# Kernel tuning notes

Hardware: AMD Instinct MI355X
Metric: run time of the kernel (lower is better)

## Reference

```python
import jax, jax.numpy as jnp
import numpy as np

TRIM = 0.2
ALPHA = 0.5
SCALES = 4
B, H, W = 64, 384, 512


def _normalize_robust(x, mask):
    # per-sample masked median shift, masked mean-abs-dev scale (MiDaS SSI norm)
    b = x.shape[0]
    xf = x.reshape(b, -1)
    mf = mask.reshape(b, -1)
    n = mf.sum(axis=1)                                   # valid count per row
    s = jnp.sort(jnp.where(mf, xf, jnp.inf), axis=1)     # masked-out -> +inf, sorted to tail
    med_idx = jnp.maximum((n - 1) // 2, 0)               # torch.median = lower median
    shift = jnp.take_along_axis(s, med_idx[:, None], axis=1)      # [b,1]
    scale = (jnp.abs(xf - shift) * mf).sum(axis=1) / n.astype(xf.dtype)
    return ((xf - shift) / scale[:, None]).reshape(x.shape)


def _gradient_loss(pred, targ):
    mask = targ > 0
    gx = jnp.abs(pred[:, :, 1:] - pred[:, :, :-1])
    gy = jnp.abs(pred[:, 1:, :] - pred[:, :-1, :])
    mx = (mask[:, :, 1:] & mask[:, :, :-1]).astype(pred.dtype)
    my = (mask[:, 1:, :] & mask[:, :-1, :]).astype(pred.dtype)
    norm = mask.sum(axis=(1, 2))
    loss = (gx * mx).sum(axis=(1, 2)) + (gy * my).sum(axis=(1, 2))
    valid = norm > 0
    loss = jnp.where(valid, loss / jnp.maximum(norm, 1).astype(pred.dtype), 0.0)
    return loss.mean()


def _multiscale_gradient_loss(pred, targ):
    total = jnp.asarray(0.0, pred.dtype)
    for scale in range(SCALES):
        step = 2 ** scale
        total = total + _gradient_loss(pred[:, ::step, ::step], targ[:, ::step, ::step])
    return total


def _trimmed_mae(pred, targ):
    b = pred.shape[0]
    p = pred.reshape(b, -1)
    t = targ.reshape(b, -1)
    n_px = p.shape[1]
    mask = t > 0
    res = jnp.where(mask, jnp.abs(p - t), 0.0)
    # NOTE: faithful to source, which indexes the UNSORTED res at max_index
    # (sorted_res is computed then never used for the threshold).
    max_index = (~mask).sum(axis=1) + int((1.0 - TRIM) * n_px)
    max_index = jnp.minimum(max_index, n_px - 1)
    thr = jnp.take_along_axis(res, max_index[:, None], axis=1)    # [b,1]
    res = jnp.where(res > thr, 0.0, res)
    norm = 2 * mask.sum(axis=1)
    valid = norm > 0
    loss = res.sum(axis=1)
    loss = jnp.where(valid, loss / jnp.maximum(norm, 1).astype(p.dtype), 0.0)
    return loss.mean()


def setup_inputs() -> dict:
    key = jax.random.key(0)
    kp, kt = jax.random.split(key)
    prediction = jax.random.normal(kp, (B, H, W), dtype=jnp.float32)
    target = jax.random.normal(kt, (B, H, W), dtype=jnp.float32)
    return {"prediction": prediction, "target": target}


def reference(prediction, target):
    mask = target > 0
    pred_n = _normalize_robust(prediction, mask)
    targ_n = _normalize_robust(target, mask)
    loss = _trimmed_mae(pred_n, targ_n)
    loss = loss + ALPHA * _multiscale_gradient_loss(pred_n, targ_n)
    return loss
```

## Files before the change

### kernel.cpp

```cpp
#include <hip/hip_runtime.h>
#include <stdint.h>

#define B 64
#define H 384
#define W 512
#define NPX (H*W)
#define TRIM_IDX 157286
#define RPW 8

#define NB1 4096
#define NBA 2048
#define NBB 512
#define CAPW 256
#define NSLOT 64
#define CAPD 8192

#define HIST_U32 (2*B*NB1)
#define ACC_OFF  HIST_U32
#define N_OFF    (ACC_OFF + 0)
#define MS_OFF   (ACC_OFF + 64)
#define TS_OFF   (ACC_OFF + 256)
#define GS_OFF   (ACC_OFF + 320)
#define TSUM_OFF (ACC_OFF + 576)
#define SB_OFF   (ACC_OFF + 704)
#define OVF_OFF  (ACC_OFF + 832)
#define ZERO_U32 (ACC_OFF + 1024)
#define K_OFF    (ACC_OFF + 1024)
#define PFX_OFF  (ACC_OFF + 1152)
#define EQ_OFF   (ACC_OFF + 1280)
#define SH_OFF   (ACC_OFF + 1408)
#define RS_OFF   (ACC_OFF + 1536)
#define THR_OFF  (ACC_OFF + 1664)
#define C2_OFF   (ACC_OFF + 1728)
#define CNT1_OFF (ACC_OFF + 1792)
#define CNTW_OFF (ACC_OFF + 1920)
#define FIX_U32  (ACC_OFF + 1920 + 2*B*NSLOT)
#define BUF_OFF  FIX_U32

__device__ __forceinline__ uint32_t fmap(float f) {
    uint32_t b = __float_as_uint(f);
    return (b & 0x80000000u) ? ~b : (b | 0x80000000u);
}
__device__ __forceinline__ float funmap(uint32_t u) {
    uint32_t b = (u & 0x80000000u) ? (u & 0x7fffffffu) : ~u;
    return __uint_as_float(b);
}

__global__ void __launch_bounds__(256) hist1_kernel(const float* __restrict__ pred,
                                                    const float* __restrict__ targ,
                                                    uint32_t* __restrict__ ws) {
    __shared__ uint32_t lh[2 * NB1];
    const int b = blockIdx.y;
    for (int i = threadIdx.x; i < 2 * NB1; i += 256) lh[i] = 0;
    __syncthreads();
    const float4* pb = (const float4*)(pred + (size_t)b * NPX);
    const float4* tb = (const float4*)(targ + (size_t)b * NPX);
    const int tid = blockIdx.x * 256 + threadIdx.x;
    uint32_t nloc = 0;
    float sump = 0.f, sumt = 0.f;
    #pragma unroll
    for (int r = 0; r < 3; r++) {
        float4 ta0 = tb[tid + (4*r+0)*4096], ta1 = tb[tid + (4*r+1)*4096];
        float4 ta2 = tb[tid + (4*r+2)*4096], ta3 = tb[tid + (4*r+3)*4096];
        float4 pa0 = pb[tid + (4*r+0)*4096], pa1 = pb[tid + (4*r+1)*4096];
        float4 pa2 = pb[tid + (4*r+2)*4096], pa3 = pb[tid + (4*r+3)*4096];
        float tA[16] = {ta0.x,ta0.y,ta0.z,ta0.w, ta1.x,ta1.y,ta1.z,ta1.w,
                        ta2.x,ta2.y,ta2.z,ta2.w, ta3.x,ta3.y,ta3.z,ta3.w};
        float pA[16] = {pa0.x,pa0.y,pa0.z,pa0.w, pa1.x,pa1.y,pa1.z,pa1.w,
                        pa2.x,pa2.y,pa2.z,pa2.w, pa3.x,pa3.y,pa3.z,pa3.w};
        #pragma unroll
        for (int e = 0; e < 16; e++) {
            float t = tA[e];
            if (t > 0.f) {
                float p = pA[e];
                nloc++; sumt += t; sump += p;
                atomicAdd(&lh[fmap(p) >> 20], 1u);
                atomicAdd(&lh[NB1 + (fmap(t) >> 20)], 1u);
            }
        }
    }
    __syncthreads();
    uint32_t* hist = ws;
    for (int i = threadIdx.x; i < 2 * NB1; i += 256) {
        uint32_t v = lh[i];
        if (v) {
            int which = i >> 12, bin = i & (NB1 - 1);
            atomicAdd(&hist[(size_t)(which * B + b) * NB1 + bin], v);
        }
    }
    for (int off = 32; off; off >>= 1) {
        nloc += __shfl_down(nloc, off, 64);
        sump += __shfl_down(sump, off, 64);
        sumt += __shfl_down(sumt, off, 64);
    }
    if ((threadIdx.x & 63) == 0) {
        if (nloc) atomicAdd(ws + N_OFF + b, nloc);
        atomicAdd(((float*)(ws + TSUM_OFF)) + b, sump);
        atomicAdd(((float*)(ws + TSUM_OFF)) + B + b, sumt);
    }
}

__global__ void select1_kernel(uint32_t* __restrict__ ws) {
    const int b = blockIdx.x, which = blockIdx.y;
    const uint32_t* h = ws + (size_t)(which * B + b) * NB1;
    const uint32_t k = (ws[N_OFF + b] - 1u) >> 1;
    const int t = threadIdx.x;
    uint32_t mysum = 0;
    #pragma unroll
    for (int i = 0; i < 16; i++) mysum += h[t * 16 + i];
    __shared__ uint32_t s[256];
    s[t] = mysum;
    __syncthreads();
    for (int off = 1; off < 256; off <<= 1) {
        uint32_t add = (t >= off) ? s[t - off] : 0u;
        __syncthreads();
        s[t] += add;
        __syncthreads();
    }
    uint32_t incl = s[t], excl = incl - mysum;
    if (k >= excl && k < incl) {
        uint32_t c = excl, bin = 0, newk = 0, e = 0;
        for (int i = 0; i < 16; i++) {
            uint32_t hv = h[t * 16 + i];
            if (k < c + hv) { bin = t * 16 + i; newk = k - c; e = hv; break; }
            c += hv;
        }
        ws[PFX_OFF + which * B + b] = bin;
        ws[K_OFF + which * B + b] = newk;
        ws[CNT1_OFF + which * B + b] = e;
    }
}

__global__ void __launch_bounds__(256) collect2_kernel(const float* __restrict__ pred,
                                                       const float* __restrict__ targ,
                                                       uint32_t* __restrict__ ws, int capw) {
    const int b = blockIdx.y;
    const int t = threadIdx.x;
    const int lane = t & 63;
    const int slot = (blockIdx.x << 2) + (t >> 6);
    const uint32_t pfxp = ws[PFX_OFF + b];
    const uint32_t pfxt = ws[PFX_OFF + B + b];
    const float4* pb = (const float4*)(pred + (size_t)b * NPX);
    const float4* tb = (const float4*)(targ + (size_t)b * NPX);
    const int tid = blockIdx.x * 256 + t;
    float* bufp = ((float*)(ws + BUF_OFF)) + ((size_t)b * NSLOT + slot) * capw;
    float* buft = ((float*)(ws + BUF_OFF)) + (((size_t)B + b) * NSLOT + slot) * capw;
    float sbp = 0.f, sbt = 0.f;
    uint32_t wp = 0, wt = 0;
    #pragma unroll
    for (int r = 0; r < 3; r++) {
        float4 ta0 = tb[tid + (4*r+0)*4096], ta1 = tb[tid + (4*r+1)*4096];
        float4 ta2 = tb[tid + (4*r+2)*4096], ta3 = tb[tid + (4*r+3)*4096];
        float4 pa0 = pb[tid + (4*r+0)*4096], pa1 = pb[tid + (4*r+1)*4096];
        float4 pa2 = pb[tid + (4*r+2)*4096], pa3 = pb[tid + (4*r+3)*4096];
        float tA[16] = {ta0.x,ta0.y,ta0.z,ta0.w, ta1.x,ta1.y,ta1.z,ta1.w,
                        ta2.x,ta2.y,ta2.z,ta2.w, ta3.x,ta3.y,ta3.z,ta3.w};
        float pA[16] = {pa0.x,pa0.y,pa0.z,pa0.w, pa1.x,pa1.y,pa1.z,pa1.w,
                        pa2.x,pa2.y,pa2.z,pa2.w, pa3.x,pa3.y,pa3.z,pa3.w};
        uint32_t mbp = 0, mbt = 0;
        #pragma unroll
        for (int e = 0; e < 16; e++) {
            float tv = tA[e], pv = pA[e];
            bool msk = tv > 0.f;
            uint32_t u1p = fmap(pv) >> 20, u1t = fmap(tv) >> 20;
            if (msk && u1p < pfxp) sbp += pv;
            if (msk && u1t < pfxt) sbt += tv;
            if (msk && u1p == pfxp) mbp |= (1u << e);
            if (msk && u1t == pfxt) mbt |= (1u << e);
        }
        uint32_t packed = (uint32_t)__popc(mbp) | ((uint32_t)__popc(mbt) << 16);
        uint32_t scan = packed;
        #pragma unroll
        for (int off = 1; off < 64; off <<= 1) {
            uint32_t v = (uint32_t)__shfl_up((int)scan, off, 64);
            if (lane >= off) scan += v;
        }
        uint32_t tot = (uint32_t)__shfl((int)scan, 63, 64);
        uint32_t exl = scan - packed;
        uint32_t op = wp + (exl & 0xFFFFu);
        uint32_t ot = wt + (exl >> 16);
        if (mbp | mbt) {
            #pragma unroll
            for (int e = 0; e < 16; e++) {
                if ((mbp >> e) & 1u) { if (op < (uint32_t)capw) bufp[op] = pA[e]; op++; }
                if ((mbt >> e) & 1u) { if (ot < (uint32_t)capw) buft[ot] = tA[e]; ot++; }
            }
        }
        wp += tot & 0xFFFFu;
        wt += tot >> 16;
    }
    if (lane == 0) {
        ws[CNTW_OFF + b * NSLOT + slot] = wp;
        ws[CNTW_OFF + (B + b) * NSLOT + slot] = wt;
        if (wp > (uint32_t)capw) ws[OVF_OFF + b] = 1u;
        if (wt > (uint32_t)capw) ws[OVF_OFF + B + b] = 1u;
    }
    for (int off = 32; off; off >>= 1) {
        sbp += __shfl_down(sbp, off, 64);
        sbt += __shfl_down(sbt, off, 64);
    }
    if (lane == 0) {
        atomicAdd(((float*)(ws + SB_OFF)) + b, sbp);
        atomicAdd(((float*)(ws + SB_OFF)) + B + b, sbt);
    }
}

__global__ void small3_kernel(const float* __restrict__ pred,
                              const float* __restrict__ targ,
                              uint32_t* __restrict__ ws, int capw) {
    const int b = blockIdx.x, which = blockIdx.y;
    const int t = threadIdx.x;
    __shared__ float dense[CAPD];
    __shared__ uint32_t cnt[NBA];
    __shared__ float fsm[NBA];
    __shared__ uint32_t sc[256];
    __shared__ float sfl[256];
    __shared__ uint32_t scnt[NSLOT], soff[NSLOT];
    __shared__ uint32_t r_bin, r_k;
    __shared__ float r_f;
    const uint32_t pfx1 = ws[PFX_OFF + which * B + b];
    const uint32_t k1 = ws[K_OFF + which * B + b];
    const uint32_t C = ws[CNT1_OFF + which * B + b];
    const bool fast = (capw > 0) && (ws[OVF_OFF + which * B + b] == 0u) && (C <= (uint32_t)CAPD);
    const uint32_t* cw = ws + CNTW_OFF + (which * B + b) * NSLOT;
    const float* bufb = ((const float*)(ws + BUF_OFF)) + ((size_t)which * B + b) * NSLOT * capw;
    const float* Tp = targ + (size_t)b * NPX;
    const float* Pp = pred + (size_t)b * NPX;

    uint32_t myc = 0;
    if (fast && t < NSLOT) myc = cw[t];
    sc[t] = myc;
    __syncthreads();
    for (int off = 1; off < NSLOT; off <<= 1) {
        uint32_t a = (t >= off) ? sc[t - off] : 0u;
        __syncthreads();
        sc[t] += a;
        __syncthreads();
    }
    if (t < NSLOT) { scnt[t] = myc; soff[t] = sc[t] - myc; }
    __syncthreads();
    if (fast) {
        const int s = t >> 2;
        const float* sb_ = bufb + (size_t)s * capw;
        const uint32_t n = scnt[s], o = soff[s];
        for (uint32_t j = (uint32_t)(t & 3); j < n; j += 4) dense[o + j] = sb_[j];
    }
    __syncthreads();

    for (int i = t; i < NBA; i += 256) { cnt[i] = 0; fsm[i] = 0.f; }
    __syncthreads();
    if (fast) {
        for (uint32_t j = t; j < C; j += 256) {
            float v = dense[j];
            uint32_t u = fmap(v), mb = (u >> 9) & (NBA - 1u);
            atomicAdd(&cnt[mb], 1u); atomicAdd(&fsm[mb], v);
        }
    } else {
        for (int j = t; j < NPX; j += 256) {
            float tvv = Tp[j];
            if (tvv > 0.f) {
                float v = (which == 0) ? Pp[j] : tvv;
                uint32_t u = fmap(v);
                if ((u >> 20) == pfx1) {
                    uint32_t mb = (u >> 9) & (NBA - 1u);
                    atomicAdd(&cnt[mb], 1u); atomicAdd(&fsm[mb], v);
                }
            }
        }
    }
    __syncthreads();
    {
        uint32_t ms = 0; float mf = 0.f;
        #pragma unroll
        for (int i = 0; i < 8; i++) { ms += cnt[t * 8 + i]; mf += fsm[t * 8 + i]; }
        sc[t] = ms; sfl[t] = mf;
        __syncthreads();
        for (int off = 1; off < 256; off <<= 1) {
            uint32_t a = (t >= off) ? sc[t - off] : 0u;
            float af = (t >= off) ? sfl[t - off] : 0.f;
            __syncthreads();
            sc[t] += a; sfl[t] += af;
            __syncthreads();
        }
        uint32_t incl = sc[t], excl = incl - ms;
        float fx = sfl[t] - mf;
        if (k1 >= excl && k1 < incl) {
            uint32_t c = excl, bin = 0, nk = 0; float f = fx;
            for (int i = 0; i < 8; i++) {
                uint32_t hv = cnt[t * 8 + i];
                if (k1 < c + hv) { bin = t * 8 + i; nk = k1 - c; break; }
                c += hv; f += fsm[t * 8 + i];
            }
            r_bin = bin; r_k = nk; r_f = f;
        }
    }
    __syncthreads();
    const uint32_t mid_sel = r_bin, k2 = r_k;
    const float fbelowA = r_f;
    __syncthreads();
    for (int i = t; i < NBB; i += 256) { cnt[i] = 0; fsm[i] = 0.f; }
    __syncthreads();
    if (fast) {
        for (uint32_t j = t; j < C; j += 256) {
            float v = dense[j];
            uint32_t u = fmap(v);
            if (((u >> 9) & (NBA - 1u)) == mid_sel) {
                uint32_t lb = u & (NBB - 1u);
                atomicAdd(&cnt[lb], 1u); atomicAdd(&fsm[lb], v);
            }
        }
    } else {
        for (int j = t; j < NPX; j += 256) {
            float tvv = Tp[j];
            if (tvv > 0.f) {
                float v = (which == 0) ? Pp[j] : tvv;
                uint32_t u = fmap(v);
                if ((u >> 20) == pfx1 && ((u >> 9) & (NBA - 1u)) == mid_sel) {
                    uint32_t lb = u & (NBB - 1u);
                    atomicAdd(&cnt[lb], 1u); atomicAdd(&fsm[lb], v);
                }
            }
        }
    }
    __syncthreads();
    {
        uint32_t ms = 0; float mf = 0.f;
        #pragma unroll
        for (int i = 0; i < 2; i++) { ms += cnt[t * 2 + i]; mf += fsm[t * 2 + i]; }
        sc[t] = ms; sfl[t] = mf;
        __syncthreads();
        for (int off = 1; off < 256; off <<= 1) {
            uint32_t a = (t >= off) ? sc[t - off] : 0u;
            float af = (t >= off) ? sfl[t - off] : 0.f;
            __syncthreads();
            sc[t] += a; sfl[t] += af;
            __syncthreads();
        }
        uint32_t incl = sc[t], excl = incl - ms;
        float fx = sfl[t] - mf;
        if (k2 >= excl && k2 < incl) {
            uint32_t c = excl, bin = 0, nk = 0, e = 0; float f = fx;
            for (int i = 0; i < 2; i++) {
                uint32_t hv = cnt[t * 2 + i];
                if (k2 < c + hv) { bin = t * 2 + i; nk = k2 - c; e = hv; break; }
                c += hv; f += fsm[t * 2 + i];
            }
            uint32_t u = (pfx1 << 20) | (mid_sel << 9) | bin;
            ((float*)(ws + SH_OFF))[which * B + b] = funmap(u);
            ws[K_OFF + which * B + b] = nk;
            ws[EQ_OFF + which * B + b] = e;
            ((float*)(ws + SB_OFF))[which * B + b] += fbelowA + f;
        }
    }
}

__global__ void param_kernel(const float* __restrict__ pred,
                             const float* __restrict__ targ,
                             uint32_t* __restrict__ ws) {
    const int b = threadIdx.x;
    if (b >= B) return;
    const uint32_t n = ws[N_OFF + b];
    const uint32_t k0 = (n - 1u) >> 1;
    float med[2], rs[2];
    uint32_t nab[2];
    #pragma unroll
    for (int w = 0; w < 2; w++) {
        float m = ((const float*)(ws + SH_OFF))[w * B + b];
        uint32_t k3 = ws[K_OFF + w * B + b];
        uint32_t e = ws[EQ_OFF + w * B + b];
        float SBv = ((const float*)(ws + SB_OFF))[w * B + b];
        float ST = ((const float*)(ws + TSUM_OFF))[w * B + b];
        uint32_t CB = k0 - k3;
        uint32_t na = n - CB - e;
        float Sab = ST - SBv - (float)e * m;
        float absdev = (Sab - (float)na * m) + ((float)CB * m - SBv);
        float scale = absdev / (float)n;
        med[w] = m; nab[w] = na;
        rs[w] = 1.f / scale;
        ((float*)(ws + RS_OFF))[w * B + b] = rs[w];
    }
    uint32_t c2 = nab[1];
    ws[C2_OFF + b] = c2;
    uint32_t mi = (uint32_t)NPX - c2 + (uint32_t)TRIM_IDX;
    if (mi > (uint32_t)(NPX - 1)) mi = NPX - 1;
    float p = pred[(size_t)b * NPX + mi];
    float t = targ[(size_t)b * NPX + mi];
    float pn = (p - med[0]) * rs[0], tn = (t - med[1]) * rs[1];
    ((float*)(ws + THR_OFF))[b] = (tn > 0.f) ? fabsf(pn - tn) : 0.f;
}

__global__ void __launch_bounds__(256) loss_kernel(const float* __restrict__ pred,
                                                   const float* __restrict__ targ,
                                                   uint32_t* __restrict__ ws) {
    const int wid = (blockIdx.x << 2) + (threadIdx.x >> 6);
    const int b = wid / (H / RPW);
    const int s0 = (wid - b * (H / RPW)) * RPW;
    const int l = threadIdx.x & 63;
    const int col = l << 3;
    const float sp = ((const float*)(ws + SH_OFF))[b];
    const float st = ((const float*)(ws + SH_OFF))[B + b];
    const float rp = ((const float*)(ws + RS_OFF))[b];
    const float rt = ((const float*)(ws + RS_OFF))[B + b];
    const float thr = ((const float*)(ws + THR_OFF))[b];
    const float* Pp = pred + (size_t)b * NPX;
    const float* Tp = targ + (size_t)b * NPX;

    const bool g1 = s0 >= 1, g2 = s0 >= 2, g4 = s0 >= 4, g8 = s0 >= 8;
    float rT[2][8], rPN[2][8];
    {
        const int roA = (g1 ? (s0 - 1) : s0) * W + col;
        const int roB = (g2 ? (s0 - 2) : s0) * W + col;
        float4 a0 = *(const float4*)(Tp + roA), a1 = *(const float4*)(Tp + roA + 4);
        float4 b0 = *(const float4*)(Pp + roA), b1 = *(const float4*)(Pp + roA + 4);
        float4 c0 = *(const float4*)(Tp + roB), c1 = *(const float4*)(Tp + roB + 4);
        float4 d0 = *(const float4*)(Pp + roB), d1 = *(const float4*)(Pp + roB + 4);
        float ta[8] = {a0.x,a0.y,a0.z,a0.w,a1.x,a1.y,a1.z,a1.w};
        float pa[8] = {b0.x,b0.y,b0.z,b0.w,b1.x,b1.y,b1.z,b1.w};
        float tc[8] = {c0.x,c0.y,c0.z,c0.w,c1.x,c1.y,c1.z,c1.w};
        float pc[8] = {d0.x,d0.y,d0.z,d0.w,d1.x,d1.y,d1.z,d1.w};
        #pragma unroll
        for (int k = 0; k < 8; k++) {
            rT[1][k] = ta[k]; rPN[1][k] = (pa[k] - sp) * rp;
            rT[0][k] = tc[k]; rPN[0][k] = (pc[k] - sp) * rp;
        }
    }

    float tl = 0.f, gl0 = 0.f, gl1 = 0.f, gl2 = 0.f, gl3 = 0.f;
    uint32_t mc = 0;

    #pragma unroll
    for (int it = 0; it < RPW; ++it) {
        const int ro = (s0 + it) * W + col;
        const int cur = it & 1, prv = cur ^ 1;
        float4 a0 = *(const float4*)(Tp + ro), a1 = *(const float4*)(Tp + ro + 4);
        float4 b0 = *(const float4*)(Pp + ro), b1 = *(const float4*)(Pp + ro + 4);
        float t[8] = {a0.x,a0.y,a0.z,a0.w,a1.x,a1.y,a1.z,a1.w};
        float p[8] = {b0.x,b0.y,b0.z,b0.w,b1.x,b1.y,b1.z,b1.w};
        float t4a = 0.f, t4b = 0.f, p4a = 0.f, p4b = 0.f, t8a = 0.f, p8a = 0.f;
        if (it == 0) {
            const int ro4 = g4 ? ro - 4 * W : ro;
            t4a = Tp[ro4]; t4b = Tp[ro4 + 4]; p4a = Pp[ro4]; p4b = Pp[ro4 + 4];
            const int ro8 = g8 ? ro - 8 * W : ro;
            t8a = Tp[ro8]; p8a = Pp[ro8];
        }
        if (it == 4) {
            const int ro4 = ro - 4 * W;
            t4a = Tp[ro4]; t4b = Tp[ro4 + 4]; p4a = Pp[ro4]; p4b = Pp[ro4 + 4];
        }
        float pn[8]; bool m[8];
        #pragma unroll
        for (int k = 0; k < 8; k++) { pn[k] = (p[k] - sp) * rp; m[k] = t[k] > st; }

        #pragma unroll
        for (int k = 0; k < 8; k++) {
            if (m[k]) {
                float tn = (t[k] - st) * rt;
                float r = fabsf(pn[k] - tn);
                if (r <= thr) tl += r;
            }
        }
        float t7p = __shfl_up(t[7], 1), pn7p = __shfl_up(pn[7], 1);
        if (l > 0 && m[0] && t7p > st) gl0 += fabsf(pn[0] - pn7p);
        #pragma unroll
        for (int k = 1; k < 8; k++) if (m[k] && m[k - 1]) gl0 += fabsf(pn[k] - pn[k - 1]);
        if (it > 0 || g1) {
            #pragma unroll
            for (int k = 0; k < 8; k++)
                if (m[k] && rT[prv][k] > st) gl0 += fabsf(pn[k] - rPN[prv][k]);
        }
        if ((it & 1) == 0) {
            float t6p = __shfl_up(t[6], 1), pn6p = __shfl_up(pn[6], 1);
            mc += (uint32_t)m[0] + m[2] + m[4] + m[6];
            if (l > 0 && m[0] && t6p > st) gl1 += fabsf(pn[0] - pn6p);
            if (m[2] && m[0]) gl1 += fabsf(pn[2] - pn[0]);
            if (m[4] && m[2]) gl1 += fabsf(pn[4] - pn[2]);
            if (m[6] && m[4]) gl1 += fabsf(pn[6] - pn[4]);
            if (it >= 2 || g2) {
                if (m[0] && rT[cur][0] > st) gl1 += fabsf(pn[0] - rPN[cur][0]);
                if (m[2] && rT[cur][2] > st) gl1 += fabsf(pn[2] - rPN[cur][2]);
                if (m[4] && rT[cur][4] > st) gl1 += fabsf(pn[4] - rPN[cur][4]);
                if (m[6] && rT[cur][6] > st) gl1 += fabsf(pn[6] - rPN[cur][6]);
            }
            if ((it & 3) == 0) {
                float t4p = __shfl_up(t[4], 1), pn4p = __shfl_up(pn[4], 1);
                mc += ((uint32_t)m[0] + m[4]) << 11;
                if (l > 0 && m[0] && t4p > st) gl2 += fabsf(pn[0] - pn4p);
                if (m[4] && m[0]) gl2 += fabsf(pn[4] - pn[0]);
                if (it == 4 || g4) {
                    if (m[0] && t4a > st) gl2 += fabsf(pn[0] - (p4a - sp) * rp);
                    if (m[4] && t4b > st) gl2 += fabsf(pn[4] - (p4b - sp) * rp);
                }
                if (it == 0) {
                    float t0p = __shfl_up(t[0], 1), pn0p = __shfl_up(pn[0], 1);
                    mc += ((uint32_t)m[0]) << 22;
                    if (l > 0 && m[0] && t0p > st) gl3 += fabsf(pn[0] - pn0p);
                    if (g8 && m[0] && t8a > st) gl3 += fabsf(pn[0] - (p8a - sp) * rp);
                }
            }
        }
        #pragma unroll
        for (int k = 0; k < 8; k++) { rT[cur][k] = t[k]; rPN[cur][k] = pn[k]; }
    }

    for (int off = 32; off; off >>= 1) {
        tl  += __shfl_down(tl, off, 64);
        gl0 += __shfl_down(gl0, off, 64);
        gl1 += __shfl_down(gl1, off, 64);
        gl2 += __shfl_down(gl2, off, 64);
        gl3 += __shfl_down(gl3, off, 64);
        mc  += __shfl_down(mc, off, 64);
    }
    if (l == 0) {
        float* gs = (float*)(ws + GS_OFF);
        atomicAdd(((float*)(ws + TS_OFF)) + b, tl);
        atomicAdd(gs + b, gl0);
        atomicAdd(gs + B + b, gl1);
        atomicAdd(gs + 2 * B + b, gl2);
        atomicAdd(gs + 3 * B + b, gl3);
        atomicAdd(ws + MS_OFF + b, mc & 0x7FFu);
        atomicAdd(ws + MS_OFF + B + b, (mc >> 11) & 0x7FFu);
        atomicAdd(ws + MS_OFF + 2 * B + b, mc >> 22);
    }
}

__global__ void finalize_kernel(const uint32_t* __restrict__ ws, float* __restrict__ out) {
    const int b = threadIdx.x;
    float v = 0.f;
    if (b < B) {
        float c2 = (float)ws[C2_OFF + b];
        const float* tsum = (const float*)(ws + TS_OFF);
        const float* gsum = (const float*)(ws + GS_OFF);
        float tm = (c2 > 0.f) ? tsum[b] / (2.f * c2) : 0.f;
        float g = (c2 > 0.f) ? gsum[b] / c2 : 0.f;
        for (int z = 0; z < 3; z++) {
            float ms = (float)ws[MS_OFF + z * B + b];
            g += (ms > 0.f) ? gsum[(1 + z) * B + b] / ms : 0.f;
        }
        v = tm + 0.5f * g;
    }
    for (int off = 32; off; off >>= 1) v += __shfl_down(v, off, 64);
    if (b == 0) out[0] = v * (1.f / 64.f);
}

extern "C" void kernel_launch(void* const* d_in, const int* in_sizes, int n_in,
                              void* d_out, int out_size, void* d_ws, size_t ws_size,
                              hipStream_t stream) {
    const float* pred = (const float*)d_in[0];
    const float* targ = (const float*)d_in[1];
    float* out = (float*)d_out;
    uint32_t* ws = (uint32_t*)d_ws;

    long avail = (long)(ws_size / 4) - (long)FIX_U32;
    int capw = 0;
    if (avail > 0) {
        long c = avail / (2L * B * NSLOT);
        capw = (int)(c < CAPW ? c : CAPW);
    }

    hipMemsetAsync(ws, 0, (size_t)ZERO_U32 * 4, stream);

    hist1_kernel<<<dim3(16, B), 256, 0, stream>>>(pred, targ, ws);
    select1_kernel<<<dim3(B, 2), 256, 0, stream>>>(ws);
    collect2_kernel<<<dim3(16, B), 256, 0, stream>>>(pred, targ, ws, capw);
    small3_kernel<<<dim3(B, 2), 256, 0, stream>>>(pred, targ, ws, capw);
    param_kernel<<<1, 64, 0, stream>>>(pred, targ, ws);
    loss_kernel<<<dim3(B * (H / RPW) / 4), 256, 0, stream>>>(pred, targ, ws);
    finalize_kernel<<<1, 64, 0, stream>>>(ws, out);
}
```

Baseline: 169.0 us.

## Replace full-pass median histogram with sampled bracket selection before collection

New measurement: 146.0 us, median of 2. 13.6% less time.

```diff
diff --git a/kernel.cpp b/kernel.cpp
--- a/kernel.cpp
+++ b/kernel.cpp
@@ -8,33 +8,32 @@
 #define TRIM_IDX 157286
 #define RPW 8
 
-#define NB1 4096
 #define NBA 2048
-#define NBB 512
 #define CAPW 256
 #define NSLOT 64
-#define CAPD 8192
-
-#define HIST_U32 (2*B*NB1)
-#define ACC_OFF  HIST_U32
-#define N_OFF    (ACC_OFF + 0)
-#define MS_OFF   (ACC_OFF + 64)
-#define TS_OFF   (ACC_OFF + 256)
-#define GS_OFF   (ACC_OFF + 320)
-#define TSUM_OFF (ACC_OFF + 576)
-#define SB_OFF   (ACC_OFF + 704)
-#define OVF_OFF  (ACC_OFF + 832)
-#define ZERO_U32 (ACC_OFF + 1024)
-#define K_OFF    (ACC_OFF + 1024)
-#define PFX_OFF  (ACC_OFF + 1152)
-#define EQ_OFF   (ACC_OFF + 1280)
-#define SH_OFF   (ACC_OFF + 1408)
-#define RS_OFF   (ACC_OFF + 1536)
-#define THR_OFF  (ACC_OFF + 1664)
-#define C2_OFF   (ACC_OFF + 1728)
-#define CNT1_OFF (ACC_OFF + 1792)
-#define CNTW_OFF (ACC_OFF + 1920)
-#define FIX_U32  (ACC_OFF + 1920 + 2*B*NSLOT)
+#define CAPD 12288
+#define SCAP 6144
+#define DELTA 0.03f
+
+#define N_OFF    0
+#define MS_OFF   64
+#define TS_OFF   256
+#define GS_OFF   320
+#define TSUM_OFF 576
+#define SB_OFF   704
+#define CB_OFF   832
+#define OVF_OFF  960
+#define ZERO_U32 1088
+#define BL_OFF   1088
+#define BH_OFF   1216
+#define K_OFF    1344
+#define EQ_OFF   1472
+#define SH_OFF   1600
+#define RS_OFF   1728
+#define THR_OFF  1856
+#define C2_OFF   1920
+#define CNTW_OFF 1984
+#define FIX_U32  (1984 + 2*B*NSLOT)
 #define BUF_OFF  FIX_U32
 
 __device__ __forceinline__ uint32_t fmap(float f) {
@@ -46,106 +45,153 @@
     return __uint_as_float(b);
 }
 
-__global__ void __launch_bounds__(256) hist1_kernel(const float* __restrict__ pred,
-                                                    const float* __restrict__ targ,
-                                                    uint32_t* __restrict__ ws) {
-    __shared__ uint32_t lh[2 * NB1];
-    const int b = blockIdx.y;
-    for (int i = threadIdx.x; i < 2 * NB1; i += 256) lh[i] = 0;
+__global__ void __launch_bounds__(1024) sample_kernel(const float* __restrict__ pred,
+                                                      const float* __restrict__ targ,
+                                                      uint32_t* __restrict__ ws) {
+    __shared__ uint32_t kp[SCAP], kt[SCAP];
+    __shared__ uint32_t h[4096];
+    __shared__ uint32_t sc[256];
+    __shared__ uint32_t s_ct, s_lo12, s_hi12, s_clo, s_bl, s_bh;
+    const int b = blockIdx.x;
+    const int t = threadIdx.x;
+    const int lane = t & 63;
+    if (t == 0) s_ct = 0;
     __syncthreads();
     const float4* pb = (const float4*)(pred + (size_t)b * NPX);
     const float4* tb = (const float4*)(targ + (size_t)b * NPX);
-    const int tid = blockIdx.x * 256 + threadIdx.x;
-    uint32_t nloc = 0;
-    float sump = 0.f, sumt = 0.f;
     #pragma unroll
-    for (int r = 0; r < 3; r++) {
-        float4 ta0 = tb[tid + (4*r+0)*4096], ta1 = tb[tid + (4*r+1)*4096];
-        float4 ta2 = tb[tid + (4*r+2)*4096], ta3 = tb[tid + (4*r+3)*4096];
-        float4 pa0 = pb[tid + (4*r+0)*4096], pa1 = pb[tid + (4*r+1)*4096];
-        float4 pa2 = pb[tid + (4*r+2)*4096], pa3 = pb[tid + (4*r+3)*4096];
-        float tA[16] = {ta0.x,ta0.y,ta0.z,ta0.w, ta1.x,ta1.y,ta1.z,ta1.w,
-                        ta2.x,ta2.y,ta2.z,ta2.w, ta3.x,ta3.y,ta3.z,ta3.w};
-        float pA[16] = {pa0.x,pa0.y,pa0.z,pa0.w, pa1.x,pa1.y,pa1.z,pa1.w,
-                        pa2.x,pa2.y,pa2.z,pa2.w, pa3.x,pa3.y,pa3.z,pa3.w};
-        #pragma unroll
-        for (int e = 0; e < 16; e++) {
-            float t = tA[e];
-            if (t > 0.f) {
-                float p = pA[e];
-                nloc++; sumt += t; sump += p;
-                atomicAdd(&lh[fmap(p) >> 20], 1u);
-                atomicAdd(&lh[NB1 + (fmap(t) >> 20)], 1u);
-            }
-        }
-    }
-    __syncthreads();
-    uint32_t* hist = ws;
-    for (int i = threadIdx.x; i < 2 * NB1; i += 256) {
-        uint32_t v = lh[i];
-        if (v) {
-            int which = i >> 12, bin = i & (NB1 - 1);
-            atomicAdd(&hist[(size_t)(which * B + b) * NB1 + bin], v);
-        }
-    }
-    for (int off = 32; off; off >>= 1) {
-        nloc += __shfl_down(nloc, off, 64);
-        sump += __shfl_down(sump, off, 64);
-        sumt += __shfl_down(sumt, off, 64);
-    }
-    if ((threadIdx.x & 63) == 0) {
-        if (nloc) atomicAdd(ws + N_OFF + b, nloc);
-        atomicAdd(((float*)(ws + TSUM_OFF)) + b, sump);
-        atomicAdd(((float*)(ws + TSUM_OFF)) + B + b, sumt);
-    }
-}
-
-__global__ void select1_kernel(uint32_t* __restrict__ ws) {
-    const int b = blockIdx.x, which = blockIdx.y;
-    const uint32_t* h = ws + (size_t)(which * B + b) * NB1;
-    const uint32_t k = (ws[N_OFF + b] - 1u) >> 1;
-    const int t = threadIdx.x;
-    uint32_t mysum = 0;
-    #pragma unroll
-    for (int i = 0; i < 16; i++) mysum += h[t * 16 + i];
-    __shared__ uint32_t s[256];
-    s[t] = mysum;
-    __syncthreads();
-    for (int off = 1; off < 256; off <<= 1) {
-        uint32_t add = (t >= off) ? s[t - off] : 0u;
+    for (int c = 0; c < 2; c++) {
+        int j = t + c * 1024;
+        int q = ((j >> 6) * 1536) + (j & 63);
+        float4 tv = tb[q], pv = pb[q];
+        float tA[4] = {tv.x, tv.y, tv.z, tv.w};
+        float pA[4] = {pv.x, pv.y, pv.z, pv.w};
+        #pragma unroll
+        for (int e = 0; e < 4; e++) {
+            bool msk = tA[e] > 0.f;
+            unsigned long long bal = __ballot(msk);
+            if (bal) {
+                int leader = __ffsll((long long)bal) - 1;
+                uint32_t base = 0;
+                if (lane == leader) base = atomicAdd(&s_ct, (uint32_t)__popcll(bal));
+                base = (uint32_t)__shfl((int)base, leader, 64);
+                if (msk) {
+                    uint32_t off = base + (uint32_t)__popcll(bal & ((1ull << lane) - 1ull));
+                    if (off < SCAP) { kt[off] = fmap(tA[e]); kp[off] = fmap(pA[e]); }
+                }
+            }
+        }
+    }
+    __syncthreads();
+    const uint32_t ct = s_ct;
+    const bool ok = (ct > 0) && (ct <= SCAP);
+    for (int w = 0; w < 2; w++) {
+        const uint32_t* K = (w == 0) ? kp : kt;
+        uint32_t BL = 0, BH = 0xFFFFFu;
+        if (ok) {
+            uint32_t rlo = (uint32_t)((0.5f - DELTA) * (float)ct);
+            uint32_t rhi = (uint32_t)((0.5f + DELTA) * (float)ct);
+            if (rhi >= ct) rhi = ct - 1;
+            for (int i = t; i < 4096; i += 1024) h[i] = 0;
+            __syncthreads();
+            for (uint32_t j = t; j < ct; j += 1024) atomicAdd(&h[K[j] >> 20], 1u);
+            __syncthreads();
+            uint32_t ms = 0;
+            if (t < 256) { for (int i = 0; i < 16; i++) ms += h[t * 16 + i]; sc[t] = ms; }
+            __syncthreads();
+            for (int off = 1; off < 256; off <<= 1) {
+                uint32_t a = (t < 256 && t >= off) ? sc[t - off] : 0u;
+                __syncthreads();
+                if (t < 256) sc[t] += a;
+                __syncthreads();
+            }
+            if (t < 256) {
+                uint32_t incl = sc[t], excl = incl - ms;
+                if (rlo >= excl && rlo < incl) {
+                    uint32_t c2 = excl;
+                    for (int i = 0; i < 16; i++) {
+                        uint32_t hv = h[t * 16 + i];
+                        if (rlo < c2 + hv) { s_lo12 = t * 16 + i; s_clo = c2; break; }
+                        c2 += hv;
+                    }
+                }
+                if (rhi >= excl && rhi < incl) {
+                    uint32_t c2 = excl;
+                    for (int i = 0; i < 16; i++) {
+                        uint32_t hv = h[t * 16 + i];
+                        if (rhi < c2 + hv) { s_hi12 = t * 16 + i; break; }
+                        c2 += hv;
+                    }
+                }
+            }
+            __syncthreads();
+            const uint32_t lo12 = s_lo12, hi12 = s_hi12, clo = s_clo;
+            const uint32_t range = (hi12 - lo12 + 1) << 8;
+            if (range > 4096) {
+                BL = lo12 << 8; BH = (hi12 << 8) | 255u;
+            } else {
+                for (int i = t; i < 4096; i += 1024) h[i] = 0;
+                __syncthreads();
+                const uint32_t base20 = lo12 << 8;
+                for (uint32_t j = t; j < ct; j += 1024) {
+                    uint32_t u = K[j], u12 = u >> 20;
+                    if (u12 >= lo12 && u12 <= hi12) atomicAdd(&h[(u >> 12) - base20], 1u);
+                }
+                __syncthreads();
+                const uint32_t r2lo = rlo - clo, r2hi = rhi - clo;
+                uint32_t ms2 = 0;
+                if (t < 256) { for (int i = 0; i < 16; i++) ms2 += h[t * 16 + i]; sc[t] = ms2; }
+                __syncthreads();
+                for (int off = 1; off < 256; off <<= 1) {
+                    uint32_t a = (t < 256 && t >= off) ? sc[t - off] : 0u;
+                    __syncthreads();
+                    if (t < 256) sc[t] += a;
+                    __syncthreads();
+                }
+                if (t < 256) {
+                    uint32_t incl = sc[t], excl = incl - ms2;
+                    if (r2lo >= excl && r2lo < incl) {
+                        uint32_t c2 = excl;
+                        for (int i = 0; i < 16; i++) {
+                            uint32_t hv = h[t * 16 + i];
+                            if (r2lo < c2 + hv) { s_bl = base20 + t * 16 + i; break; }
+                            c2 += hv;
+                        }
+                    }
+                    if (r2hi >= excl && r2hi < incl) {
+                        uint32_t c2 = excl;
+                        for (int i = 0; i < 16; i++) {
+                            uint32_t hv = h[t * 16 + i];
+                            if (r2hi < c2 + hv) { s_bh = base20 + t * 16 + i; break; }
+                            c2 += hv;
+                        }
+                    }
+                }
+                __syncthreads();
+                BL = s_bl; BH = s_bh;
+            }
+        }
+        if (t == 0) { ws[BL_OFF + w * B + b] = BL; ws[BH_OFF + w * B + b] = BH; }
         __syncthreads();
-        s[t] += add;
-        __syncthreads();
-    }
-    uint32_t incl = s[t], excl = incl - mysum;
-    if (k >= excl && k < incl) {
-        uint32_t c = excl, bin = 0, newk = 0, e = 0;
-        for (int i = 0; i < 16; i++) {
-            uint32_t hv = h[t * 16 + i];
-            if (k < c + hv) { bin = t * 16 + i; newk = k - c; e = hv; break; }
-            c += hv;
-        }
-        ws[PFX_OFF + which * B + b] = bin;
-        ws[K_OFF + which * B + b] = newk;
-        ws[CNT1_OFF + which * B + b] = e;
-    }
-}
-
-__global__ void __launch_bounds__(256) collect2_kernel(const float* __restrict__ pred,
-                                                       const float* __restrict__ targ,
-                                                       uint32_t* __restrict__ ws, int capw) {
+    }
+}
+
+__global__ void __launch_bounds__(256) collect_kernel(const float* __restrict__ pred,
+                                                      const float* __restrict__ targ,
+                                                      uint32_t* __restrict__ ws, int capw) {
     const int b = blockIdx.y;
     const int t = threadIdx.x;
     const int lane = t & 63;
     const int slot = (blockIdx.x << 2) + (t >> 6);
-    const uint32_t pfxp = ws[PFX_OFF + b];
-    const uint32_t pfxt = ws[PFX_OFF + B + b];
+    const uint32_t BLp = ws[BL_OFF + b],     BHp = ws[BH_OFF + b];
+    const uint32_t BLt = ws[BL_OFF + B + b], BHt = ws[BH_OFF + B + b];
     const float4* pb = (const float4*)(pred + (size_t)b * NPX);
     const float4* tb = (const float4*)(targ + (size_t)b * NPX);
     const int tid = blockIdx.x * 256 + t;
     float* bufp = ((float*)(ws + BUF_OFF)) + ((size_t)b * NSLOT + slot) * capw;
     float* buft = ((float*)(ws + BUF_OFF)) + (((size_t)B + b) * NSLOT + slot) * capw;
-    float sbp = 0.f, sbt = 0.f;
+    float sbp = 0.f, sbt = 0.f, sump = 0.f, sumt = 0.f;
+    uint32_t nloc = 0, cbp = 0, cbt = 0;
     uint32_t wp = 0, wt = 0;
     #pragma unroll
     for (int r = 0; r < 3; r++) {
@@ -161,12 +207,14 @@
         #pragma unroll
         for (int e = 0; e < 16; e++) {
             float tv = tA[e], pv = pA[e];
-            bool msk = tv > 0.f;
-            uint32_t u1p = fmap(pv) >> 20, u1t = fmap(tv) >> 20;
-            if (msk && u1p < pfxp) sbp += pv;
-            if (msk && u1t < pfxt) sbt += tv;
-            if (msk && u1p == pfxp) mbp |= (1u << e);
-            if (msk && u1t == pfxt) mbt |= (1u << e);
+            if (tv > 0.f) {
+                nloc++; sumt += tv; sump += pv;
+                uint32_t up = fmap(pv) >> 12, ut = fmap(tv) >> 12;
+                if (up < BLp) { cbp++; sbp += pv; }
+                else if (up <= BHp) mbp |= (1u << e);
+                if (ut < BLt) { cbt++; sbt += tv; }
+                else if (ut <= BHt) mbt |= (1u << e);
+            }
         }
         uint32_t packed = (uint32_t)__popc(mbp) | ((uint32_t)__popc(mbt) << 16);
         uint32_t scan = packed;
@@ -196,12 +244,22 @@
         if (wt > (uint32_t)capw) ws[OVF_OFF + B + b] = 1u;
     }
     for (int off = 32; off; off >>= 1) {
-        sbp += __shfl_down(sbp, off, 64);
-        sbt += __shfl_down(sbt, off, 64);
+        nloc += __shfl_down(nloc, off, 64);
+        sump += __shfl_down(sump, off, 64);
+        sumt += __shfl_down(sumt, off, 64);
+        sbp  += __shfl_down(sbp, off, 64);
+        sbt  += __shfl_down(sbt, off, 64);
+        cbp  += __shfl_down(cbp, off, 64);
+        cbt  += __shfl_down(cbt, off, 64);
     }
     if (lane == 0) {
+        if (nloc) atomicAdd(ws + N_OFF + b, nloc);
+        atomicAdd(((float*)(ws + TSUM_OFF)) + b, sump);
+        atomicAdd(((float*)(ws + TSUM_OFF)) + B + b, sumt);
         atomicAdd(((float*)(ws + SB_OFF)) + b, sbp);
         atomicAdd(((float*)(ws + SB_OFF)) + B + b, sbt);
+        if (cbp) atomicAdd(ws + CB_OFF + b, cbp);
+        if (cbt) atomicAdd(ws + CB_OFF + B + b, cbt);
     }
 }
 
@@ -211,24 +269,22 @@
     const int b = blockIdx.x, which = blockIdx.y;
     const int t = threadIdx.x;
     __shared__ float dense[CAPD];
-    __shared__ uint32_t cnt[NBA];
-    __shared__ float fsm[NBA];
+    __shared__ uint32_t cnt[4096];
+    __shared__ float fsm[4096];
     __shared__ uint32_t sc[256];
     __shared__ float sfl[256];
     __shared__ uint32_t scnt[NSLOT], soff[NSLOT];
-    __shared__ uint32_t r_bin, r_k;
-    __shared__ float r_f;
-    const uint32_t pfx1 = ws[PFX_OFF + which * B + b];
-    const uint32_t k1 = ws[K_OFF + which * B + b];
-    const uint32_t C = ws[CNT1_OFF + which * B + b];
-    const bool fast = (capw > 0) && (ws[OVF_OFF + which * B + b] == 0u) && (C <= (uint32_t)CAPD);
+    __shared__ uint32_t r_bin, r_k, s_Ctot;
+    __shared__ float r_f, s_facc;
+    const uint32_t n = ws[N_OFF + b];
+    const uint32_t k0 = (n - 1u) >> 1;
+    const uint32_t CBv = ws[CB_OFF + which * B + b];
     const uint32_t* cw = ws + CNTW_OFF + (which * B + b) * NSLOT;
     const float* bufb = ((const float*)(ws + BUF_OFF)) + ((size_t)which * B + b) * NSLOT * capw;
     const float* Tp = targ + (size_t)b * NPX;
     const float* Pp = pred + (size_t)b * NPX;
 
-    uint32_t myc = 0;
-    if (fast && t < NSLOT) myc = cw[t];
+    uint32_t myc = (t < NSLOT) ? cw[t] : 0u;
     sc[t] = myc;
     __syncthreads();
     for (int off = 1; off < NSLOT; off <<= 1) {
@@ -238,22 +294,82 @@
         __syncthreads();
     }
     if (t < NSLOT) { scnt[t] = myc; soff[t] = sc[t] - myc; }
-    __syncthreads();
+    if (t == NSLOT - 1) s_Ctot = sc[t];
+    __syncthreads();
+    const uint32_t Ctot = s_Ctot;
+    const long k_in = (long)k0 - (long)CBv;
+    const bool fast = (capw > 0) && (ws[OVF_OFF + which * B + b] == 0u) &&
+                      (Ctot <= (uint32_t)CAPD) && (k_in >= 0) && (k_in < (long)Ctot);
     if (fast) {
         const int s = t >> 2;
         const float* sb_ = bufb + (size_t)s * capw;
-        const uint32_t n = scnt[s], o = soff[s];
-        for (uint32_t j = (uint32_t)(t & 3); j < n; j += 4) dense[o + j] = sb_[j];
-    }
+        const uint32_t nn = scnt[s], o = soff[s];
+        for (uint32_t j = (uint32_t)(t & 3); j < nn; j += 4) dense[o + j] = sb_[j];
+    }
+    __syncthreads();
+
+    uint32_t kr = fast ? (uint32_t)k_in : k0;
+
+    for (int i = t; i < 4096; i += 256) { cnt[i] = 0; fsm[i] = 0.f; }
+    __syncthreads();
+    if (fast) {
+        for (uint32_t j = t; j < Ctot; j += 256) {
+            float v = dense[j];
+            uint32_t key = fmap(v) >> 20;
+            atomicAdd(&cnt[key], 1u); atomicAdd(&fsm[key], v);
+        }
+    } else {
+        for (int j = t; j < NPX; j += 256) {
+            float tvv = Tp[j];
+            if (tvv > 0.f) {
+                float v = (which == 0) ? Pp[j] : tvv;
+                uint32_t key = fmap(v) >> 20;
+                atomicAdd(&cnt[key], 1u); atomicAdd(&fsm[key], v);
+            }
+        }
+    }
+    __syncthreads();
+    {
+        uint32_t ms = 0; float mf = 0.f;
+        #pragma unroll
+        for (int i = 0; i < 16; i++) { ms += cnt[t * 16 + i]; mf += fsm[t * 16 + i]; }
+        sc[t] = ms; sfl[t] = mf;
+        __syncthreads();
+        for (int off = 1; off < 256; off <<= 1) {
+            uint32_t a = (t >= off) ? sc[t - off] : 0u;
+            float af = (t >= off) ? sfl[t - off] : 0.f;
+            __syncthreads();
+            sc[t] += a; sfl[t] += af;
+            __syncthreads();
+        }
+        uint32_t incl = sc[t], excl = incl - ms;
+        float fx = sfl[t] - mf;
+        if (kr >= excl && kr < incl) {
+            uint32_t c = excl, bin = 0, nk = 0; float f = fx;
+            for (int i = 0; i < 16; i++) {
+                uint32_t hv = cnt[t * 16 + i];
+                if (kr < c + hv) { bin = t * 16 + i; nk = kr - c; break; }
+                c += hv; f += fsm[t * 16 + i];
+            }
+            r_bin = bin; r_k = nk; r_f = f;
+        }
+    }
+    __syncthreads();
+    const uint32_t sel0 = r_bin;
+    kr = r_k;
+    if (t == 0) s_facc = r_f;
     __syncthreads();
 
     for (int i = t; i < NBA; i += 256) { cnt[i] = 0; fsm[i] = 0.f; }
     __syncthreads();
     if (fast) {
-        for (uint32_t j = t; j < C; j += 256) {
+        for (uint32_t j = t; j < Ctot; j += 256) {
             float v = dense[j];
-            uint32_t u = fmap(v), mb = (u >> 9) & (NBA - 1u);
-            atomicAdd(&cnt[mb], 1u); atomicAdd(&fsm[mb], v);
+            uint32_t u = fmap(v);
+            if ((u >> 20) == sel0) {
+                uint32_t key = (u >> 9) & (NBA - 1u);
+                atomicAdd(&cnt[key], 1u); atomicAdd(&fsm[key], v);
+            }
         }
     } else {
         for (int j = t; j < NPX; j += 256) {
@@ -261,9 +377,9 @@
             if (tvv > 0.f) {
                 float v = (which == 0) ? Pp[j] : tvv;
                 uint32_t u = fmap(v);
-                if ((u >> 20) == pfx1) {
-                    uint32_t mb = (u >> 9) & (NBA - 1u);
-                    atomicAdd(&cnt[mb], 1u); atomicAdd(&fsm[mb], v);
+                if ((u >> 20) == sel0) {
+                    uint32_t key = (u >> 9) & (NBA - 1u);
+                    atomicAdd(&cnt[key], 1u); atomicAdd(&fsm[key], v);
                 }
             }
         }
@@ -284,29 +400,31 @@
         }
         uint32_t incl = sc[t], excl = incl - ms;
         float fx = sfl[t] - mf;
-        if (k1 >= excl && k1 < incl) {
+        if (kr >= excl && kr < incl) {
             uint32_t c = excl, bin = 0, nk = 0; float f = fx;
             for (int i = 0; i < 8; i++) {
                 uint32_t hv = cnt[t * 8 + i];
-                if (k1 < c + hv) { bin = t * 8 + i; nk = k1 - c; break; }
+                if (kr < c + hv) { bin = t * 8 + i; nk = kr - c; break; }
                 c += hv; f += fsm[t * 8 + i];
             }
             r_bin = bin; r_k = nk; r_f = f;
         }
     }
     __syncthreads();
-    const uint32_t mid_sel = r_bin, k2 = r_k;
-    const float fbelowA = r_f;
-    __syncthreads();
-    for (int i = t; i < NBB; i += 256) { cnt[i] = 0; fsm[i] = 0.f; }
+    const uint32_t pfx23 = (sel0 << 11) | r_bin;
+    kr = r_k;
+    if (t == 0) s_facc += r_f;
+    __syncthreads();
+
+    for (int i = t; i < 512; i += 256) { cnt[i] = 0; fsm[i] = 0.f; }
     __syncthreads();
     if (fast) {
-        for (uint32_t j = t; j < C; j += 256) {
+        for (uint32_t j = t; j < Ctot; j += 256) {
             float v = dense[j];
             uint32_t u = fmap(v);
-            if (((u >> 9) & (NBA - 1u)) == mid_sel) {
-                uint32_t lb = u & (NBB - 1u);
-                atomicAdd(&cnt[lb], 1u); atomicAdd(&fsm[lb], v);
+            if ((u >> 9) == pfx23) {
+                uint32_t key = u & 511u;
+                atomicAdd(&cnt[key], 1u); atomicAdd(&fsm[key], v);
             }
         }
     } else {
@@ -315,9 +433,9 @@
             if (tvv > 0.f) {
                 float v = (which == 0) ? Pp[j] : tvv;
                 uint32_t u = fmap(v);
-                if ((u >> 20) == pfx1 && ((u >> 9) & (NBA - 1u)) == mid_sel) {
-                    uint32_t lb = u & (NBB - 1u);
-                    atomicAdd(&cnt[lb], 1u); atomicAdd(&fsm[lb], v);
+                if ((u >> 9) == pfx23) {
+                    uint32_t key = u & 511u;
+                    atomicAdd(&cnt[key], 1u); atomicAdd(&fsm[key], v);
                 }
             }
         }
@@ -338,18 +456,20 @@
         }
         uint32_t incl = sc[t], excl = incl - ms;
         float fx = sfl[t] - mf;
-        if (k2 >= excl && k2 < incl) {
+        if (kr >= excl && kr < incl) {
             uint32_t c = excl, bin = 0, nk = 0, e = 0; float f = fx;
             for (int i = 0; i < 2; i++) {
                 uint32_t hv = cnt[t * 2 + i];
-                if (k2 < c + hv) { bin = t * 2 + i; nk = k2 - c; e = hv; break; }
+                if (kr < c + hv) { bin = t * 2 + i; nk = kr - c; e = hv; break; }
                 c += hv; f += fsm[t * 2 + i];
             }
-            uint32_t u = (pfx1 << 20) | (mid_sel << 9) | bin;
+            uint32_t u = (pfx23 << 9) | bin;
             ((float*)(ws + SH_OFF))[which * B + b] = funmap(u);
             ws[K_OFF + which * B + b] = nk;
             ws[EQ_OFF + which * B + b] = e;
-            ((float*)(ws + SB_OFF))[which * B + b] += fbelowA + f;
+            float* sb = ((float*)(ws + SB_OFF)) + which * B + b;
+            float below = s_facc + f;
+            *sb = fast ? (*sb + below) : below;
         }
     }
 }
@@ -559,9 +679,8 @@
 
     hipMemsetAsync(ws, 0, (size_t)ZERO_U32 * 4, stream);
 
-    hist1_kernel<<<dim3(16, B), 256, 0, stream>>>(pred, targ, ws);
-    select1_kernel<<<dim3(B, 2), 256, 0, stream>>>(ws);
-    collect2_kernel<<<dim3(16, B), 256, 0, stream>>>(pred, targ, ws, capw);
+    sample_kernel<<<dim3(B), 1024, 0, stream>>>(pred, targ, ws);
+    collect_kernel<<<dim3(16, B), 256, 0, stream>>>(pred, targ, ws, capw);
     small3_kernel<<<dim3(B, 2), 256, 0, stream>>>(pred, targ, ws, capw);
     param_kernel<<<1, 64, 0, stream>>>(pred, targ, ws);
     loss_kernel<<<dim3(B * (H / RPW) / 4), 256, 0, stream>>>(pred, targ, ws);
```
